# Kernel optimization log

Hardware: AMD Instinct MI355X
Metric: run time of the kernel (lower is better)

Reference implementation:

```python
import jax, jax.numpy as jnp
import numpy as np

N_NODES = 20000
N_REL = 8
N_EDGES = 320000
IN_DIM, HID_DIM, OUT_DIM = 1280, 512, 256


def _rgcn_layer(x, W, root, bias, src, dst, etype):
    """PyG RGCNConv with num_bases=None, aggr='mean' (mean per (node, relation)).
    x: [N, in], W: [R, in, out], root: [in, out], bias: [out].
    """
    n = x.shape[0]
    # per-(dst, relation) in-degree for relation-wise mean
    key = dst * N_REL + etype  # [E]
    counts = jax.ops.segment_sum(jnp.ones(etype.shape, x.dtype), key,
                                 num_segments=n * N_REL)
    deg = jnp.maximum(counts[key], 1.0)  # [E]
    # transform once per relation, then gather per edge
    H = jnp.einsum('ni,rio->rno', x, W)          # [R, N, out]
    msg = H[etype, src] / deg[:, None]           # [E, out]
    agg = jax.ops.segment_sum(msg, dst, num_segments=n)  # [N, out]
    return agg + x @ root + bias


def setup_inputs() -> dict:
    key = jax.random.key(0)
    ks = jax.random.split(key, 9)
    x = jax.random.normal(ks[0], (N_NODES, IN_DIM), dtype=jnp.float32)
    edge_index = jax.random.randint(ks[1], (2, N_EDGES), 0, N_NODES, dtype=jnp.int32)
    edge_type = jax.random.randint(ks[2], (N_EDGES,), 0, N_REL, dtype=jnp.int32)
    s1 = 1.0 / np.sqrt(IN_DIM)
    s2 = 1.0 / np.sqrt(HID_DIM)
    return {
        'x': x,
        'edge_index': edge_index,
        'edge_type': edge_type,
        'W1': jax.random.normal(ks[3], (N_REL, IN_DIM, HID_DIM), dtype=jnp.float32) * s1,
        'root1': jax.random.normal(ks[4], (IN_DIM, HID_DIM), dtype=jnp.float32) * s1,
        'b1': jnp.zeros((HID_DIM,), dtype=jnp.float32),
        'W2': jax.random.normal(ks[5], (N_REL, HID_DIM, OUT_DIM), dtype=jnp.float32) * s2,
        'root2': jax.random.normal(ks[6], (HID_DIM, OUT_DIM), dtype=jnp.float32) * s2,
        'b2': jnp.zeros((OUT_DIM,), dtype=jnp.float32),
    }


def reference(x, edge_index, edge_type, W1, root1, b1, W2, root2, b2):
    src, dst = edge_index[0], edge_index[1]
    h = _rgcn_layer(x, W1, root1, b1, src, dst, edge_type)
    h = jax.nn.relu(h)
    # dropout is identity in eval mode
    out = _rgcn_layer(h, W2, root2, b2, src, dst, edge_type)
    return out
```

## Files before the change

kernel.cpp:

```cpp
#include <hip/hip_runtime.h>
#include <hip/hip_bf16.h>

#define N_REL 8

typedef unsigned short ushort_t;
typedef unsigned int uint_t;
typedef __attribute__((ext_vector_type(8))) short short8;
typedef __attribute__((ext_vector_type(4))) float floatx4;

static __device__ __forceinline__ ushort_t f2bf(float f) {
    union { float f; unsigned u; } v; v.f = f;
    unsigned r = v.u + 0x7fff + ((v.u >> 16) & 1);
    return (ushort_t)(r >> 16);
}

typedef __attribute__((address_space(1))) void glob_void;
typedef __attribute__((address_space(3))) void lds_void;

static __device__ __forceinline__ void load_lds16(const void* g, void* l) {
    __builtin_amdgcn_global_load_lds((glob_void*)g, (lds_void*)l, 16, 0, 0);
}

static __device__ __forceinline__ void stage_half(const ushort_t* __restrict__ g,
                                                  int row0, int rmax, int K, int k0,
                                                  ushort_t* lds, int w, int l) {
    const int rl = l >> 3;
    const int gc = ((l & 7) ^ rl) * 8;
#pragma unroll
    for (int s = 0; s < 2; ++s) {
        int r = row0 + s * 64 + w * 8 + rl;
        r = r < rmax ? r : rmax - 1;
        load_lds16(g + (size_t)r * K + k0 + gc, lds + (s * 64 + w * 8) * 64);
    }
}


__global__ __launch_bounds__(256) void hist_kernel(const int* __restrict__ dst,
                                                   const int* __restrict__ et,
                                                   int* __restrict__ cnt, int E) {
    int e = blockIdx.x * blockDim.x + threadIdx.x;
    if (e < E) atomicAdd(&cnt[dst[e] * N_REL + et[e]], 1);
}

__global__ __launch_bounds__(256) void scan1(const int* __restrict__ cnt,
                                             int* __restrict__ off,
                                             int* __restrict__ bsum, int nk) {
    __shared__ int s[256];
    int t = threadIdx.x;
    int k = blockIdx.x * 256 + t;
    int v = k < nk ? cnt[k] : 0;
    s[t] = v; __syncthreads();
    for (int d = 1; d < 256; d <<= 1) {
        int x = (t >= d) ? s[t - d] : 0;
        __syncthreads(); s[t] += x; __syncthreads();
    }
    if (k < nk) off[k] = s[t] - v;
    if (t == 255) bsum[blockIdx.x] = s[255];
}

__global__ __launch_bounds__(1024) void scan2(int* __restrict__ bsum, int nb) {
    __shared__ int s[1024];
    int t = threadIdx.x;
    int v = t < nb ? bsum[t] : 0;
    s[t] = v; __syncthreads();
    for (int d = 1; d < 1024; d <<= 1) {
        int x = (t >= d) ? s[t - d] : 0;
        __syncthreads(); s[t] += x; __syncthreads();
    }
    if (t < nb) bsum[t] = s[t] - v;
}

__global__ __launch_bounds__(256) void scan3(int* __restrict__ off,
                                             const int* __restrict__ bsum,
                                             int* __restrict__ cursor,
                                             int nk) {
    int k = blockIdx.x * 256 + threadIdx.x;
    if (k >= nk) return;
    int o = off[k] + bsum[k >> 8];
    off[k] = o;
    cursor[k] = o;
}

__global__ __launch_bounds__(256) void scatter_desc(const int* __restrict__ dst,
                                                    const int* __restrict__ et,
                                                    const int* __restrict__ src,
                                                    const int* __restrict__ cnt,
                                                    int* __restrict__ cursor,
                                                    uint2* __restrict__ edesc, int E) {
    int e = blockIdx.x * blockDim.x + threadIdx.x;
    if (e < E) {
        int key = dst[e] * N_REL + et[e];
        int pos = atomicAdd(&cursor[key], 1);
        float inv = 1.0f / (float)cnt[key];
        edesc[pos] = make_uint2((uint_t)src[e] | ((uint_t)et[e] << 27),
                                __float_as_uint(inv));
    }
}


__global__ __launch_bounds__(256) void cast_bf16(const float* __restrict__ in,
                                                 ushort_t* __restrict__ out, long n) {
    long idx = ((long)blockIdx.x * blockDim.x + threadIdx.x) * 4;
    if (idx + 4 <= n) {
        float4 v = *(const float4*)(in + idx);
        ushort_t o[4] = {f2bf(v.x), f2bf(v.y), f2bf(v.z), f2bf(v.w)};
        *(uint2*)(out + idx) = *(const uint2*)o;
    } else {
        for (; idx < n; ++idx) out[idx] = f2bf(in[idx]);
    }
}

__global__ __launch_bounds__(256) void transpose_cast(const float* __restrict__ in,
                                                      ushort_t* __restrict__ out,
                                                      int K, int N) {
    __shared__ float tile[32][33];
    const float* inp = in + (size_t)blockIdx.z * K * N;
    ushort_t* outp = out + (size_t)blockIdx.z * K * N;
    int n0 = blockIdx.x * 32, k0 = blockIdx.y * 32;
    int tx = threadIdx.x & 31, ty = threadIdx.x >> 5;
#pragma unroll
    for (int s = 0; s < 4; ++s)
        tile[ty + 8 * s][tx] = inp[(size_t)(k0 + ty + 8 * s) * N + n0 + tx];
    __syncthreads();
#pragma unroll
    for (int s = 0; s < 4; ++s)
        outp[(size_t)(n0 + ty + 8 * s) * K + k0 + tx] = f2bf(tile[tx][ty + 8 * s]);
}


#define STAGE_A(b, h, ktx) stage_half(A, bm + (h) * 128, M, K, ((ktx) << 6), &sh.st[(b)][0][(h)][0], w, l)
#define STAGE_B(b, h, ktx) stage_half(Bt, bn + (h) * 128, N, K, ((ktx) << 6), &sh.st[(b)][1][(h)][0], w, l)

#define LOAD_A(b, qm)                                                          \
    {                                                                          \
        const ushort_t* pa_ = &sh.st[(b)][0][(qm)][0];                         \
        _Pragma("unroll") for (int i_ = 0; i_ < 4; ++i_) {                     \
            const int r_ = wm * 64 + i_ * 16 + l16;                            \
            _Pragma("unroll") for (int kk_ = 0; kk_ < 2; ++kk_) {              \
                const int ch_ = (kk_ * 4 + quad) ^ (r_ & 7);                   \
                areg[i_][kk_] = *(const short8*)&pa_[r_ * 64 + ch_ * 8];       \
            }                                                                  \
        }                                                                      \
    }

#define LOAD_B(b, qn)                                                          \
    {                                                                          \
        const ushort_t* pb_ = &sh.st[(b)][1][(qn)][0];                         \
        _Pragma("unroll") for (int j_ = 0; j_ < 2; ++j_) {                     \
            const int r_ = wn * 32 + j_ * 16 + l16;                            \
            _Pragma("unroll") for (int kk_ = 0; kk_ < 2; ++kk_) {              \
                const int ch_ = (kk_ * 4 + quad) ^ (r_ & 7);                   \
                breg[(qn)][j_][kk_] = *(const short8*)&pb_[r_ * 64 + ch_ * 8]; \
            }                                                                  \
        }                                                                      \
    }

#define MFMA_Q(qm, qn)                                                              \
    _Pragma("unroll") for (int i_ = 0; i_ < 4; ++i_)                                \
        _Pragma("unroll") for (int j_ = 0; j_ < 2; ++j_)                            \
            _Pragma("unroll") for (int kk_ = 0; kk_ < 2; ++kk_)                     \
                acc[(qm)][(qn)][i_][j_] = __builtin_amdgcn_mfma_f32_16x16x32_bf16(  \
                    areg[i_][kk_], breg[(qn)][j_][kk_], acc[(qm)][(qn)][i_][j_], 0, 0, 0);

#define PHASE_SYNC()                                                           \
    __builtin_amdgcn_s_barrier();                                              \
    asm volatile("s_waitcnt lgkmcnt(0)" ::: "memory");                         \
    __builtin_amdgcn_sched_barrier(0)

#define WINDOW(kt, b)                                                          \
    {                                                                          \
                                 \
        LOAD_A(b, 0);                                                          \
        LOAD_B(b, 0);                                                          \
        if ((kt) + 1 < nkt) STAGE_A((b) ^ 1, 1, (kt) + 1);                     \
        PHASE_SYNC();                                                          \
        __builtin_amdgcn_s_setprio(1);                                         \
        MFMA_Q(0, 0);                                                          \
        __builtin_amdgcn_s_setprio(0);                                         \
        __builtin_amdgcn_s_barrier();                                          \
                        \
        LOAD_B(b, 1);                                                          \
        if ((kt) + 2 < nkt) STAGE_A(b, 0, (kt) + 2);                           \
        PHASE_SYNC();                                                          \
        __builtin_amdgcn_s_setprio(1);                                         \
        MFMA_Q(0, 1);                                                          \
        __builtin_amdgcn_s_setprio(0);                                         \
        __builtin_amdgcn_s_barrier();                                          \
                            \
        LOAD_A(b, 1);                                                          \
        if ((kt) + 2 < nkt) STAGE_B(b, 0, (kt) + 2);                           \
        PHASE_SYNC();                                                          \
        __builtin_amdgcn_s_setprio(1);                                         \
        MFMA_Q(1, 0);                                                          \
        __builtin_amdgcn_s_setprio(0);                                         \
        __builtin_amdgcn_s_barrier();                                          \
           \
        if ((kt) + 2 < nkt) {                                                  \
            STAGE_B(b, 1, (kt) + 2);                                           \
            asm volatile("s_waitcnt vmcnt(6)" ::: "memory");                   \
        } else {                                                               \
            asm volatile("s_waitcnt vmcnt(0)" ::: "memory");  \
        }                                                                      \
        __builtin_amdgcn_s_barrier();                                          \
        __builtin_amdgcn_sched_barrier(0);                                     \
        __builtin_amdgcn_s_setprio(1);                                         \
        MFMA_Q(1, 1);                                                          \
        __builtin_amdgcn_s_setprio(0);                                         \
        __builtin_amdgcn_s_barrier();                                          \
    }

__global__ __launch_bounds__(512, 2) void gemm256(const ushort_t* __restrict__ A,
                                                  const ushort_t* __restrict__ Bt,
                                                  ushort_t* __restrict__ C,
                                                  int M, int K, int N) {
    __shared__ union {
        __align__(16) ushort_t st[2][2][2][128 * 64];
        __align__(16) ushort_t c[256 * 256];
    } sh;

    const int t = threadIdx.x;
    const int l = t & 63;
    const int w = t >> 6;
    const int wm = w >> 2, wn = w & 3;
    const int quad = l >> 4, l16 = l & 15;

    const int nx = gridDim.x;
    const int nwg = nx * gridDim.y;
    const int orig = blockIdx.y * nx + blockIdx.x;
    const int q8 = nwg >> 3, r8 = nwg & 7;
    const int xcd = orig & 7;
    const int wgid = ((xcd < r8) ? xcd * (q8 + 1) : r8 * (q8 + 1) + (xcd - r8) * q8) + (orig >> 3);
    const int bm = (wgid / nx) * 256;
    const int bn = (wgid % nx) * 256;

    const int nkt = K >> 6;

    floatx4 acc[2][2][4][2];
#pragma unroll
    for (int a = 0; a < 2; ++a)
#pragma unroll
        for (int bq = 0; bq < 2; ++bq)
#pragma unroll
            for (int i = 0; i < 4; ++i)
#pragma unroll
                for (int j = 0; j < 2; ++j) acc[a][bq][i][j] = (floatx4)(0.f);

    short8 areg[4][2];
    short8 breg[2][2][2];

    STAGE_A(0, 0, 0); STAGE_B(0, 0, 0); STAGE_B(0, 1, 0); STAGE_A(0, 1, 0);
    STAGE_A(1, 0, 1); STAGE_B(1, 0, 1); STAGE_B(1, 1, 1);
    asm volatile("s_waitcnt vmcnt(6)" ::: "memory");
    __builtin_amdgcn_s_barrier();

    for (int kt = 0; kt < nkt; kt += 2) {
        WINDOW(kt, 0);
        WINDOW(kt + 1, 1);
    }

    __syncthreads();
#pragma unroll
    for (int qm = 0; qm < 2; ++qm)
#pragma unroll
        for (int qn = 0; qn < 2; ++qn)
#pragma unroll
            for (int i = 0; i < 4; ++i)
#pragma unroll
                for (int j = 0; j < 2; ++j) {
                    const int rl = qm * 128 + wm * 64 + i * 16 + quad * 4;
                    const int cl = qn * 128 + wn * 32 + j * 16 + l16;
#pragma unroll
                    for (int rg = 0; rg < 4; ++rg)
                        sh.c[(rl + rg) * 256 + cl] = f2bf(acc[qm][qn][i][j][rg]);
                }
    __syncthreads();
#pragma unroll
    for (int sw = 0; sw < 16; ++sw) {
        const int idx = sw * 512 + t;
        const int row = idx >> 5;
        const int ch = (idx & 31) * 8;
        const int grow = bm + row;
        if (grow < M)
            *(uint4*)(C + (size_t)grow * N + bn + ch) = *(const uint4*)&sh.c[row * 256 + ch];
    }
}

#undef STAGE_A
#undef STAGE_B
#undef LOAD_A
#undef LOAD_B
#undef MFMA_Q
#undef PHASE_SYNC
#undef WINDOW


template <int DIM, bool L1MODE>
__global__ __launch_bounds__(128) void segsum_wave2(const ushort_t* __restrict__ H,
                                                    const float* __restrict__ bias,
                                                    const int* __restrict__ off,
                                                    const int* __restrict__ cnt,
                                                    const uint2* __restrict__ edesc,
                                                    ushort_t* __restrict__ outb,
                                                    float* __restrict__ outf) {
    constexpr int VPT = DIM / 64;
    constexpr int WPT = VPT / 2;
    const int d = blockIdx.x;
    const int lane = threadIdx.x & 63;
    const int wv = threadIdx.x >> 6;
    const int hs = (N_REL + 1) * DIM;
    __shared__ float red[DIM];

    const int base = off[d * N_REL];
    const int total = off[d * N_REL + N_REL - 1] + cnt[d * N_REL + N_REL - 1] - base;
    int h = ((total >> 1) + 7) & ~7;
    if (h > total) h = total;
    const int start = wv ? h : 0;
    const int end = wv ? total : h;

    float acc[VPT];
    if (wv == 0) {
        uint_t rw[WPT];
        const ushort_t* hp = H + (size_t)d * hs + VPT * lane;
        if constexpr (WPT == 4) *(uint4*)rw = *(const uint4*)hp;
        else                    *(uint2*)rw = *(const uint2*)hp;
#pragma unroll
        for (int jq = 0; jq < WPT; ++jq) {
            acc[2 * jq]     = __uint_as_float(rw[jq] << 16);
            acc[2 * jq + 1] = __uint_as_float(rw[jq] & 0xffff0000u);
        }
        const float* bp = bias + VPT * lane;
#pragma unroll
        for (int jq = 0; jq < VPT; ++jq) acc[jq] += bp[jq];
    } else {
#pragma unroll
        for (int jq = 0; jq < VPT; ++jq) acc[jq] = 0.f;
    }

    const uint2* __restrict__ ed = edesc + base;
    const ushort_t* __restrict__ Hlane = H + VPT * lane;

    int p = start;
    while (p + 8 <= end) {
        uint2 dsc[8];
#pragma unroll
        for (int q = 0; q < 8; ++q) dsc[q] = ed[p + q];
        uint_t val[8][WPT];
#pragma unroll
        for (int q = 0; q < 8; ++q) {
            const uint_t pk = dsc[q].x;
            const size_t s = pk & 0x07ffffffu;
            const int r = pk >> 27;
            const ushort_t* hp = Hlane + s * hs + (r + 1) * DIM;
            if constexpr (WPT == 4) *(uint4*)val[q] = *(const uint4*)hp;
            else                    *(uint2*)val[q] = *(const uint2*)hp;
        }
#pragma unroll
        for (int q = 0; q < 8; ++q) {
            const float inv = __uint_as_float(dsc[q].y);
#pragma unroll
            for (int jq = 0; jq < WPT; ++jq) {
                acc[2 * jq]     += inv * __uint_as_float(val[q][jq] << 16);
                acc[2 * jq + 1] += inv * __uint_as_float(val[q][jq] & 0xffff0000u);
            }
        }
        p += 8;
    }
    for (; p < end; ++p) {
        const uint2 dq = ed[p];
        const uint_t pk = dq.x;
        const size_t s = pk & 0x07ffffffu;
        const int r = pk >> 27;
        const float inv = __uint_as_float(dq.y);
        uint_t vw[WPT];
        const ushort_t* hp = Hlane + s * hs + (r + 1) * DIM;
        if constexpr (WPT == 4) *(uint4*)vw = *(const uint4*)hp;
        else                    *(uint2*)vw = *(const uint2*)hp;
#pragma unroll
        for (int jq = 0; jq < WPT; ++jq) {
            acc[2 * jq]     += inv * __uint_as_float(vw[jq] << 16);
            acc[2 * jq + 1] += inv * __uint_as_float(vw[jq] & 0xffff0000u);
        }
    }

    if (wv == 1) {
#pragma unroll
        for (int jq = 0; jq < VPT; ++jq) red[VPT * lane + jq] = acc[jq];
    }
    __syncthreads();
    if (wv == 0) {
#pragma unroll
        for (int jq = 0; jq < VPT; ++jq) acc[jq] += red[VPT * lane + jq];

        if constexpr (L1MODE) {
            ushort_t ob[VPT];
#pragma unroll
            for (int jq = 0; jq < VPT; ++jq) ob[jq] = f2bf(fmaxf(acc[jq], 0.f));
            if constexpr (WPT == 4)
                *(uint4*)(outb + (size_t)d * DIM + VPT * lane) = *(const uint4*)ob;
            else
                *(uint2*)(outb + (size_t)d * DIM + VPT * lane) = *(const uint2*)ob;
        } else {
            float* op = outf + (size_t)d * DIM + VPT * lane;
#pragma unroll
            for (int jq = 0; jq < WPT; ++jq)
                *(float2*)(op + 2 * jq) = make_float2(acc[2 * jq], acc[2 * jq + 1]);
        }
    }
}


extern "C" void kernel_launch(void* const* d_in, const int* in_sizes, int n_in,
                              void* d_out, int out_size, void* d_ws, size_t ws_size,
                              hipStream_t stream) {
    const float* x     = (const float*)d_in[0];
    const int*   eidx  = (const int*)d_in[1];
    const int*   etype = (const int*)d_in[2];
    const float* W1    = (const float*)d_in[3];
    const float* root1 = (const float*)d_in[4];
    const float* b1    = (const float*)d_in[5];
    const float* W2    = (const float*)d_in[6];
    const float* root2 = (const float*)d_in[7];
    const float* b2    = (const float*)d_in[8];
    float* out = (float*)d_out;

    const int IN_DIM = 1280, HID_DIM = 512, OUT_DIM = 256;
    const int E = in_sizes[2];
    const int N = in_sizes[0] / IN_DIM;
    const int NK = N * N_REL;
    const int* srcs = eidx;
    const int* dsts = eidx + E;

    char* ws = (char*)d_ws;
    size_t offb = 0;
    auto alloc = [&](size_t bytes) { void* p = ws + offb; offb += (bytes + 255) & ~(size_t)255; return p; };
    int*      cnt    = (int*)alloc((size_t)NK * 4);
    int*      off    = (int*)alloc((size_t)NK * 4);
    int*      cursor = (int*)alloc((size_t)NK * 4);
    int*      bsum   = (int*)alloc(1024 * 4);
    uint2*    edesc  = (uint2*)alloc((size_t)E * 8);
    ushort_t* x_bf   = (ushort_t*)alloc((size_t)N * IN_DIM * 2);
    ushort_t* rW1t   = (ushort_t*)alloc((size_t)(N_REL + 1) * IN_DIM * HID_DIM * 2);
    ushort_t* r1t    = rW1t;
    ushort_t* W1t    = rW1t + (size_t)HID_DIM * IN_DIM;
    ushort_t* rW2t   = (ushort_t*)alloc((size_t)(N_REL + 1) * HID_DIM * OUT_DIM * 2);
    ushort_t* r2t    = rW2t;
    ushort_t* W2t    = rW2t + (size_t)OUT_DIM * HID_DIM;
    ushort_t* Hb     = (ushort_t*)alloc((size_t)N * (N_REL + 1) * HID_DIM * 2);
    ushort_t* hb_bf  = x_bf;
    (void)ws_size;

    const int nb = (NK + 255) / 256;

    hipMemsetAsync(cnt, 0, (size_t)NK * 4, stream);
    hist_kernel<<<(E + 255) / 256, 256, 0, stream>>>(dsts, etype, cnt, E);
    scan1<<<nb, 256, 0, stream>>>(cnt, off, bsum, NK);
    scan2<<<1, 1024, 0, stream>>>(bsum, nb);
    scan3<<<nb, 256, 0, stream>>>(off, bsum, cursor, NK);
    scatter_desc<<<(E + 255) / 256, 256, 0, stream>>>(dsts, etype, srcs, cnt, cursor, edesc, E);

    {
        long n = (long)N * IN_DIM;
        cast_bf16<<<(unsigned)((n / 4 + 255) / 256), 256, 0, stream>>>(x, x_bf, n);
    }
    transpose_cast<<<dim3(HID_DIM / 32, IN_DIM / 32, 1), 256, 0, stream>>>(root1, r1t, IN_DIM, HID_DIM);
    transpose_cast<<<dim3(HID_DIM / 32, IN_DIM / 32, N_REL), 256, 0, stream>>>(W1, W1t, IN_DIM, HID_DIM);
    transpose_cast<<<dim3(OUT_DIM / 32, HID_DIM / 32, 1), 256, 0, stream>>>(root2, r2t, HID_DIM, OUT_DIM);
    transpose_cast<<<dim3(OUT_DIM / 32, HID_DIM / 32, N_REL), 256, 0, stream>>>(W2, W2t, HID_DIM, OUT_DIM);

    const int mb = (N + 255) / 256;

    {
        const int NTOT = (N_REL + 1) * HID_DIM;
        gemm256<<<dim3(NTOT / 256, mb), 512, 0, stream>>>(x_bf, rW1t, Hb, N, IN_DIM, NTOT);
        segsum_wave2<512, true><<<N, 128, 0, stream>>>(Hb, b1, off, cnt, edesc, hb_bf, nullptr);
    }

    {
        const int NTOT = (N_REL + 1) * OUT_DIM;
        gemm256<<<dim3(NTOT / 256, mb), 512, 0, stream>>>(hb_bf, rW2t, Hb, N, HID_DIM, NTOT);
        segsum_wave2<256, false><<<N, 128, 0, stream>>>(Hb, b2, off, cnt, edesc, nullptr, out);
    }
}
```

Before: 613.9 us.

## Split per-relation transform and aggregation into three chunks to shrink H buffer

Replaces the single wide GEMM over root plus all eight relations and one aggregation pass with three GEMM and segment-sum pairs, each covering three relation column blocks. Partial sums accumulate in an fp32 node buffer, and the final chunk applies ReLU and casts to bf16. The aim is to keep the intermediate H buffer (a third of its former size) more cache-resident during the random gathers, at the cost of more launches, extra read-modify-write passes over the output, and smaller GEMM grids.

```diff
diff --git a/kernel.cpp b/kernel.cpp
--- a/kernel.cpp
+++ b/kernel.cpp
@@ -169,7 +169,6 @@
 
 #define WINDOW(kt, b)                                                          \
     {                                                                          \
-                                 \
         LOAD_A(b, 0);                                                          \
         LOAD_B(b, 0);                                                          \
         if ((kt) + 1 < nkt) STAGE_A((b) ^ 1, 1, (kt) + 1);                     \
@@ -178,7 +177,6 @@
         MFMA_Q(0, 0);                                                          \
         __builtin_amdgcn_s_setprio(0);                                         \
         __builtin_amdgcn_s_barrier();                                          \
-                        \
         LOAD_B(b, 1);                                                          \
         if ((kt) + 2 < nkt) STAGE_A(b, 0, (kt) + 2);                           \
         PHASE_SYNC();                                                          \
@@ -186,7 +184,6 @@
         MFMA_Q(0, 1);                                                          \
         __builtin_amdgcn_s_setprio(0);                                         \
         __builtin_amdgcn_s_barrier();                                          \
-                            \
         LOAD_A(b, 1);                                                          \
         if ((kt) + 2 < nkt) STAGE_B(b, 0, (kt) + 2);                           \
         PHASE_SYNC();                                                          \
@@ -194,7 +191,6 @@
         MFMA_Q(1, 0);                                                          \
         __builtin_amdgcn_s_setprio(0);                                         \
         __builtin_amdgcn_s_barrier();                                          \
-           \
         if ((kt) + 2 < nkt) {                                                  \
             STAGE_B(b, 1, (kt) + 2);                                           \
             asm volatile("s_waitcnt vmcnt(6)" ::: "memory");                   \
@@ -294,31 +290,33 @@
 #undef WINDOW
 
 
-template <int DIM, bool L1MODE>
-__global__ __launch_bounds__(128) void segsum_wave2(const ushort_t* __restrict__ H,
+template <int DIM, int MODE>
+__global__ __launch_bounds__(128) void segsum_chunk(const ushort_t* __restrict__ H,
                                                     const float* __restrict__ bias,
                                                     const int* __restrict__ off,
                                                     const int* __restrict__ cnt,
                                                     const uint2* __restrict__ edesc,
+                                                    float* __restrict__ outf,
                                                     ushort_t* __restrict__ outb,
-                                                    float* __restrict__ outf) {
+                                                    int rlo, int rhi, int hs) {
     constexpr int VPT = DIM / 64;
     constexpr int WPT = VPT / 2;
     const int d = blockIdx.x;
     const int lane = threadIdx.x & 63;
     const int wv = threadIdx.x >> 6;
-    const int hs = (N_REL + 1) * DIM;
     __shared__ float red[DIM];
 
-    const int base = off[d * N_REL];
-    const int total = off[d * N_REL + N_REL - 1] + cnt[d * N_REL + N_REL - 1] - base;
+    const int base = off[d * N_REL + rlo];
+    const int total = off[d * N_REL + rhi] + cnt[d * N_REL + rhi] - base;
     int h = ((total >> 1) + 7) & ~7;
     if (h > total) h = total;
     const int start = wv ? h : 0;
     const int end = wv ? total : h;
 
     float acc[VPT];
-    if (wv == 0) {
+#pragma unroll
+    for (int jq = 0; jq < VPT; ++jq) acc[jq] = 0.f;
+    if (MODE == 0 && wv == 0) {
         uint_t rw[WPT];
         const ushort_t* hp = H + (size_t)d * hs + VPT * lane;
         if constexpr (WPT == 4) *(uint4*)rw = *(const uint4*)hp;
@@ -331,11 +329,9 @@
         const float* bp = bias + VPT * lane;
 #pragma unroll
         for (int jq = 0; jq < VPT; ++jq) acc[jq] += bp[jq];
-    } else {
-#pragma unroll
-        for (int jq = 0; jq < VPT; ++jq) acc[jq] = 0.f;
-    }
-
+    }
+
+    const int colbase = (MODE == 0) ? DIM : 0;
     const uint2* __restrict__ ed = edesc + base;
     const ushort_t* __restrict__ Hlane = H + VPT * lane;
 
@@ -349,8 +345,8 @@
         for (int q = 0; q < 8; ++q) {
             const uint_t pk = dsc[q].x;
             const size_t s = pk & 0x07ffffffu;
-            const int r = pk >> 27;
-            const ushort_t* hp = Hlane + s * hs + (r + 1) * DIM;
+            const int co = ((int)(pk >> 27) - rlo) * DIM + colbase;
+            const ushort_t* hp = Hlane + s * hs + co;
             if constexpr (WPT == 4) *(uint4*)val[q] = *(const uint4*)hp;
             else                    *(uint2*)val[q] = *(const uint2*)hp;
         }
@@ -369,10 +365,10 @@
         const uint2 dq = ed[p];
         const uint_t pk = dq.x;
         const size_t s = pk & 0x07ffffffu;
-        const int r = pk >> 27;
+        const int co = ((int)(pk >> 27) - rlo) * DIM + colbase;
         const float inv = __uint_as_float(dq.y);
         uint_t vw[WPT];
-        const ushort_t* hp = Hlane + s * hs + (r + 1) * DIM;
+        const ushort_t* hp = Hlane + s * hs + co;
         if constexpr (WPT == 4) *(uint4*)vw = *(const uint4*)hp;
         else                    *(uint2*)vw = *(const uint2*)hp;
 #pragma unroll
@@ -391,19 +387,30 @@
 #pragma unroll
         for (int jq = 0; jq < VPT; ++jq) acc[jq] += red[VPT * lane + jq];
 
-        if constexpr (L1MODE) {
+        if constexpr (MODE == 0) {
+            float* op = outf + (size_t)d * DIM + VPT * lane;
+#pragma unroll
+            for (int jq = 0; jq < WPT; ++jq)
+                *(float2*)(op + 2 * jq) = make_float2(acc[2 * jq], acc[2 * jq + 1]);
+        } else if constexpr (MODE == 1) {
+            float* op = outf + (size_t)d * DIM + VPT * lane;
+#pragma unroll
+            for (int jq = 0; jq < WPT; ++jq) {
+                float2 g = *(float2*)(op + 2 * jq);
+                g.x += acc[2 * jq];
+                g.y += acc[2 * jq + 1];
+                *(float2*)(op + 2 * jq) = g;
+            }
+        } else {
+            const float* ip = outf + (size_t)d * DIM + VPT * lane;
             ushort_t ob[VPT];
 #pragma unroll
-            for (int jq = 0; jq < VPT; ++jq) ob[jq] = f2bf(fmaxf(acc[jq], 0.f));
+            for (int jq = 0; jq < VPT; ++jq)
+                ob[jq] = f2bf(fmaxf(ip[jq] + acc[jq], 0.f));
             if constexpr (WPT == 4)
                 *(uint4*)(outb + (size_t)d * DIM + VPT * lane) = *(const uint4*)ob;
             else
                 *(uint2*)(outb + (size_t)d * DIM + VPT * lane) = *(const uint2*)ob;
-        } else {
-            float* op = outf + (size_t)d * DIM + VPT * lane;
-#pragma unroll
-            for (int jq = 0; jq < WPT; ++jq)
-                *(float2*)(op + 2 * jq) = make_float2(acc[2 * jq], acc[2 * jq + 1]);
         }
     }
 }
@@ -445,7 +452,8 @@
     ushort_t* rW2t   = (ushort_t*)alloc((size_t)(N_REL + 1) * HID_DIM * OUT_DIM * 2);
     ushort_t* r2t    = rW2t;
     ushort_t* W2t    = rW2t + (size_t)OUT_DIM * HID_DIM;
-    ushort_t* Hb     = (ushort_t*)alloc((size_t)N * (N_REL + 1) * HID_DIM * 2);
+    ushort_t* Hb     = (ushort_t*)alloc((size_t)N * 3 * HID_DIM * 2);
+    float*    hbuf   = (float*)alloc((size_t)N * HID_DIM * 4);
     ushort_t* hb_bf  = x_bf;
     (void)ws_size;
 
@@ -470,14 +478,22 @@
     const int mb = (N + 255) / 256;
 
     {
-        const int NTOT = (N_REL + 1) * HID_DIM;
-        gemm256<<<dim3(NTOT / 256, mb), 512, 0, stream>>>(x_bf, rW1t, Hb, N, IN_DIM, NTOT);
-        segsum_wave2<512, true><<<N, 128, 0, stream>>>(Hb, b1, off, cnt, edesc, hb_bf, nullptr);
+        const int HS = 3 * HID_DIM;
+        gemm256<<<dim3(HS / 256, mb), 512, 0, stream>>>(x_bf, rW1t, Hb, N, IN_DIM, HS);
+        segsum_chunk<512, 0><<<N, 128, 0, stream>>>(Hb, b1, off, cnt, edesc, hbuf, nullptr, 0, 1, HS);
+        gemm256<<<dim3(HS / 256, mb), 512, 0, stream>>>(x_bf, rW1t + (size_t)HS * IN_DIM, Hb, N, IN_DIM, HS);
+        segsum_chunk<512, 1><<<N, 128, 0, stream>>>(Hb, nullptr, off, cnt, edesc, hbuf, nullptr, 2, 4, HS);
+        gemm256<<<dim3(HS / 256, mb), 512, 0, stream>>>(x_bf, rW1t + (size_t)2 * HS * IN_DIM, Hb, N, IN_DIM, HS);
+        segsum_chunk<512, 2><<<N, 128, 0, stream>>>(Hb, nullptr, off, cnt, edesc, hbuf, hb_bf, 5, 7, HS);
     }
 
     {
-        const int NTOT = (N_REL + 1) * OUT_DIM;
-        gemm256<<<dim3(NTOT / 256, mb), 512, 0, stream>>>(hb_bf, rW2t, Hb, N, HID_DIM, NTOT);
-        segsum_wave2<256, false><<<N, 128, 0, stream>>>(Hb, b2, off, cnt, edesc, nullptr, out);
-    }
-}
+        const int HS = 3 * OUT_DIM;
+        gemm256<<<dim3(HS / 256, mb), 512, 0, stream>>>(hb_bf, rW2t, Hb, N, HID_DIM, HS);
+        segsum_chunk<256, 0><<<N, 128, 0, stream>>>(Hb, b2, off, cnt, edesc, out, nullptr, 0, 1, HS);
+        gemm256<<<dim3(HS / 256, mb), 512, 0, stream>>>(hb_bf, rW2t + (size_t)HS * HID_DIM, Hb, N, HID_DIM, HS);
+        segsum_chunk<256, 1><<<N, 128, 0, stream>>>(Hb, nullptr, off, cnt, edesc, out, nullptr, 2, 4, HS);
+        gemm256<<<dim3(HS / 256, mb), 512, 0, stream>>>(hb_bf, rW2t + (size_t)2 * HS * HID_DIM, Hb, N, HID_DIM, HS);
+        segsum_chunk<256, 1><<<N, 128, 0, stream>>>(Hb, nullptr, off, cnt, edesc, out, nullptr, 5, 7, HS);
+    }
+}
```

New measurement: 701.3 us. +14.3%, slower.
